# Optimization experiments

Hardware: AMD Instinct MI355X
Metric: run time of the kernel (lower is better)

The kernel has to match this reference:

```python
import jax, jax.numpy as jnp
import numpy as np

P, R, C, K = 128, 256, 256, 3  # nplants, nrows, ncols, kernel_size


def _gconv(x, w, b, groups):
    # x: (1, Cin, R, C); w: (Cout, Cin//groups, K, K); SAME pad == k//2 torch pad for odd k
    y = jax.lax.conv_general_dilated(
        x, w, window_strides=(1, 1), padding='SAME',
        dimension_numbers=('NCHW', 'OIHW', 'NCHW'),
        feature_group_count=groups)
    return y + b[None, :, None, None]


def setup_inputs() -> dict:
    key = jax.random.key(0)
    ks = jax.random.split(key, 10)
    sc = 1.0 / np.sqrt(2 * K * K)  # torch Conv2d default init scale (fan_in = 2*K*K per group)
    return {
        "inputs": jax.random.normal(ks[0], (P, R, C), jnp.float32),
        "prev_state": jax.random.normal(ks[1], (P, R, C), jnp.float32),
        "w_reset": jax.random.uniform(ks[2], (P, 2, K, K), jnp.float32, -sc, sc),
        "b_reset": jax.random.uniform(ks[3], (P,), jnp.float32, -sc, sc),
        "w_update": jax.random.uniform(ks[4], (P, 2, K, K), jnp.float32, -sc, sc),
        "b_update": jax.random.uniform(ks[5], (P,), jnp.float32, -sc, sc),
        "w_out": jax.random.uniform(ks[6], (P, 2, K, K), jnp.float32, -sc, sc),
        "b_out": jax.random.uniform(ks[7], (P,), jnp.float32, -sc, sc),
        # per-pixel reduce weight: Conv2d(R*C*P -> R*C, 1x1, groups=R*C) weight reshaped to (R, C, P)
        "w_read": jax.random.uniform(ks[8], (R, C, P), jnp.float32, -1.0 / np.sqrt(P), 1.0 / np.sqrt(P)),
        "bias": jax.random.normal(ks[9], (R, C), jnp.float32),
    }


def reference(inputs, prev_state, w_reset, b_reset, w_update, b_update,
              w_out, b_out, w_read, bias):
    x = inputs[None]        # (1, P, R, C)
    h = prev_state[None]    # (1, P, R, C)
    stacked = jnp.concatenate([x, h], axis=1)  # (1, 2P, R, C)
    update = jax.nn.sigmoid(_gconv(stacked, w_update, b_update, P))
    reset = jax.nn.sigmoid(_gconv(stacked, w_reset, b_reset, P))
    cand = jnp.tanh(_gconv(jnp.concatenate([x, h * reset], axis=1), w_out, b_out, P))
    new_state = h * (1.0 - update) + cand * update  # (1, P, R, C)
    # grouped 1x1 conv == per-pixel dot over plants
    out = jnp.einsum('prc,rcp->rc', new_state[0], w_read) + bias  # (R, C)
    return out
```

## Files before the change

kernel.cpp:

```cpp
#include <hip/hip_runtime.h>

#define PCNT 128
#define RCdim 256
#define IMG (RCdim*RCdim)
#define PITCH 42
#define TROWS 36
#define TELEMS (TROWS*PITCH)
#define NSLOT 360
#define NTHREADS 256
#define NTASK (34*9)

__device__ __forceinline__ float sig_(float x){ return 1.0f/(1.0f+__expf(-x)); }
__device__ __forceinline__ float th_(float x){ float e=__expf(2.0f*x); return 1.0f-2.0f/(e+1.0f); }

__device__ __forceinline__ void stage4(const float* __restrict__ src, float* __restrict__ dst,
                                       int R0, int C0, int tid){
#pragma unroll
  for (int j=0;j<2;++j){
    int s = j*NTHREADS + tid;
    if (s < NSLOT){
      int rr = s/10, q = s - rr*10;
      int gr = R0-2+rr, gc = C0-4+4*q;
      float4 v = make_float4(0.f,0.f,0.f,0.f);
      if ((unsigned)gr < 256u && (unsigned)gc < 253u)
        v = *(const float4*)(src + gr*RCdim + gc);
      float* d = dst + rr*PITCH + 4*q;
      *(float2*)(d  ) = make_float2(v.x, v.y);
      *(float2*)(d+2) = make_float2(v.z, v.w);
    }
  }
}

__device__ __forceinline__ void load8(const float* __restrict__ T, int row0, int col0, float v[3][8]){
#pragma unroll
  for (int dy=0;dy<3;++dy){
    const float2* p = (const float2*)&T[(row0+dy)*PITCH + col0];
    float2 a=p[0],b=p[1],c=p[2],d=p[3];
    v[dy][0]=a.x; v[dy][1]=a.y; v[dy][2]=b.x; v[dy][3]=b.y;
    v[dy][4]=c.x; v[dy][5]=c.y; v[dy][6]=d.x; v[dy][7]=d.y;
  }
}

template<int OFF>
__device__ __forceinline__ void conv_acc(const float v[3][8], const float w9[9], float o[4]){
#pragma unroll
  for (int ky=0; ky<3; ++ky)
#pragma unroll
    for (int kx=0; kx<3; ++kx){
      const float w = w9[ky*3+kx];
#pragma unroll
      for (int k=0;k<4;++k) o[k] = fmaf(w, v[ky][k+kx+OFF], o[k]);
    }
}

__device__ __forceinline__ void load_w18(const float* __restrict__ g, float w0[9], float w1[9]){
#pragma unroll
  for (int i=0;i<9;++i){ w0[i]=g[i]; w1[i]=g[9+i]; }
}

__device__ __forceinline__ void hr_compute(float (*sm)[TELEMS],
    const float* __restrict__ w_reset, const float* __restrict__ b_reset,
    int a, int tid, float ga[2][4], float gb[2][4]){
  float wr0[9],wr1[9],ws0[9],ws1[9];
  load_w18(w_reset + a*18,     wr0, wr1);
  load_w18(w_reset + (a+1)*18, ws0, ws1);
  const float bra = b_reset[a], brb = b_reset[a+1];
#pragma unroll
  for (int j=0;j<2;++j){
    int sIdx = j*NTHREADS + tid;
    if (sIdx < NTASK){
      int row = sIdx/9, s = sIdx - row*9;
      int rr = row + 1, col0 = 4*s;
      float va[3][8], vb[3][8];
      load8(sm[0], rr-1, col0, va);
      load8(sm[1], rr-1, col0, vb);
      float ra[4] = {bra,bra,bra,bra};
      conv_acc<2>(va, wr0, ra); conv_acc<2>(vb, wr1, ra);
      load8(sm[2], rr-1, col0, va);
      load8(sm[3], rr-1, col0, vb);
      float rb[4] = {brb,brb,brb,brb};
      conv_acc<2>(va, ws0, rb); conv_acc<2>(vb, ws1, rb);
#pragma unroll
      for (int k=0;k<4;++k){ ga[j][k]=sig_(ra[k]); gb[j][k]=sig_(rb[k]); }
    }
  }
}

__device__ __forceinline__ void hr_write(float (*sm)[TELEMS], int tid,
    const float ga[2][4], const float gb[2][4]){
#pragma unroll
  for (int j=0;j<2;++j){
    int sIdx = j*NTHREADS + tid;
    if (sIdx < NTASK){
      int row = sIdx/9, s = sIdx - row*9;
      int rr = row + 1, col0 = 4*s;
      int cnt = (s==8) ? 2 : 4;
      for (int k=0;k<cnt;++k){
        int o = rr*PITCH + col0 + 3 + k;
        sm[0][o] = sm[4][o] * ga[j][k];
        sm[2][o] = sm[5][o] * gb[j][k];
      }
    }
  }
}

__global__ void init_out(const float* __restrict__ bias, float* __restrict__ out){
  int i = blockIdx.x * NTHREADS + threadIdx.x;
  out[i] = bias[i];
}

__global__ void __launch_bounds__(NTHREADS)
reduce_out(const float* __restrict__ ns, const float* __restrict__ w_read,
           const float* __restrict__ bias, float* __restrict__ out){
  const int px = blockIdx.x * NTHREADS + threadIdx.x;
  float acc = bias[px];
  const float* wr = w_read + (size_t)px * PCNT;
#pragma unroll 4
  for (int p0 = 0; p0 < PCNT; p0 += 4){
    const float4 w4 = *(const float4*)&wr[p0];
    acc = fmaf(ns[(size_t)(p0  )*IMG + px], w4.x,
          fmaf(ns[(size_t)(p0+1)*IMG + px], w4.y,
          fmaf(ns[(size_t)(p0+2)*IMG + px], w4.z,
          fmaf(ns[(size_t)(p0+3)*IMG + px], w4.w, acc))));
  }
  out[px] = acc;
}

template<bool SPLIT>
__global__ void __launch_bounds__(NTHREADS, 4)
gru_fused(const float* __restrict__ x, const float* __restrict__ h,
          const float* __restrict__ w_reset, const float* __restrict__ b_reset,
          const float* __restrict__ w_update, const float* __restrict__ b_update,
          const float* __restrict__ w_out, const float* __restrict__ b_out,
          const float* __restrict__ w_read, float* __restrict__ ws,
          float* __restrict__ out)
{
  __shared__ float sm[6][TELEMS];
  const int tid  = threadIdx.x;
  const int bid  = blockIdx.x;
  const int pg   = bid & 15;
  const int tile = bid >> 4;
  const int R0 = (tile >> 3) * 32;
  const int C0 = (tile & 7) * 32;
  const int trow = tid >> 3;
  const int tcol = (tid & 7) * 4;
  const int gidx = (R0 + trow) * RCdim + C0 + tcol;

  float acc[4] = {0.f,0.f,0.f,0.f};
  float v0[3][8], v1[3][8];

#pragma unroll 1
  for (int t = 0; t < 2; ++t){
    const int a  = 4*pg + 2*t;
    const int ph = 64 + 2*pg + t;
    __syncthreads();
    stage4(x + (size_t)(2*a  )*IMG, sm[0], R0,C0,tid);
    stage4(x + (size_t)(2*a+1)*IMG, sm[1], R0,C0,tid);
    stage4(x + (size_t)(2*a+2)*IMG, sm[2], R0,C0,tid);
    stage4(x + (size_t)(2*a+3)*IMG, sm[3], R0,C0,tid);
    stage4(h + (size_t)(a    )*IMG, sm[4], R0,C0,tid);
    stage4(h + (size_t)(a+1  )*IMG, sm[5], R0,C0,tid);
    __syncthreads();

    float hc0[4], hc1[4], uH[4];
    {
      float wa[9], wb[9];
      load_w18(w_update + ph*18, wa, wb);
      const float b = b_update[ph];
      float uo[4] = {b,b,b,b};
      load8(sm[4], trow+1, tcol+2, v0);
      load8(sm[5], trow+1, tcol+2, v1);
      conv_acc<1>(v0, wa, uo); conv_acc<1>(v1, wb, uo);
#pragma unroll
      for (int k=0;k<4;++k){ hc0[k]=v0[1][k+2]; hc1[k]=v1[1][k+2]; uH[k]=sig_(uo[k]); }
    }
    float ns0[4], ns1[4];
    {
      float wua[9],wub[9],woa[9],wob[9];
      load_w18(w_update + a*18, wua, wub);
      load_w18(w_out    + a*18, woa, wob);
      const float bu=b_update[a], bo=b_out[a];
      float uo[4]={bu,bu,bu,bu}, co[4]={bo,bo,bo,bo};
      load8(sm[0], trow+1, tcol+2, v0);
      load8(sm[1], trow+1, tcol+2, v1);
      conv_acc<1>(v0, wua, uo); conv_acc<1>(v1, wub, uo);
      conv_acc<1>(v0, woa, co); conv_acc<1>(v1, wob, co);
#pragma unroll
      for (int k=0;k<4;++k){ float u=sig_(uo[k]); ns0[k]=hc0[k]+u*(th_(co[k])-hc0[k]); }
    }
    {
      float wua[9],wub[9],woa[9],wob[9];
      load_w18(w_update + (a+1)*18, wua, wub);
      load_w18(w_out    + (a+1)*18, woa, wob);
      const float bu=b_update[a+1], bo=b_out[a+1];
      float uo[4]={bu,bu,bu,bu}, co[4]={bo,bo,bo,bo};
      load8(sm[2], trow+1, tcol+2, v0);
      load8(sm[3], trow+1, tcol+2, v1);
      conv_acc<1>(v0, wua, uo); conv_acc<1>(v1, wub, uo);
      conv_acc<1>(v0, woa, co); conv_acc<1>(v1, wob, co);
#pragma unroll
      for (int k=0;k<4;++k){ float u=sig_(uo[k]); ns1[k]=hc1[k]+u*(th_(co[k])-hc1[k]); }
    }
    if (SPLIT){
      *(float4*)&ws[(size_t)a    *IMG + gidx] = make_float4(ns0[0],ns0[1],ns0[2],ns0[3]);
      *(float4*)&ws[(size_t)(a+1)*IMG + gidx] = make_float4(ns1[0],ns1[1],ns1[2],ns1[3]);
    } else {
#pragma unroll
      for (int k=0;k<4;++k){
        const float2 wv = *(const float2*)&w_read[(size_t)(gidx+k)*PCNT + a];
        acc[k] = fmaf(ns0[k], wv.x, fmaf(ns1[k], wv.y, acc[k]));
      }
    }
    float ga[2][4], gb[2][4];
    hr_compute(sm, w_reset, b_reset, a, tid, ga, gb);
    __syncthreads();
    hr_write(sm, tid, ga, gb);
    __syncthreads();
    {
      float woa[9], wob[9];
      load_w18(w_out + ph*18, woa, wob);
      const float bo = b_out[ph];
      float co[4]={bo,bo,bo,bo};
      load8(sm[0], trow+1, tcol+2, v0);
      load8(sm[2], trow+1, tcol+2, v1);
      conv_acc<1>(v0, woa, co); conv_acc<1>(v1, wob, co);
      const float4 hp4 = *(const float4*)&h[(size_t)ph*IMG + gidx];
      const float hp[4] = {hp4.x,hp4.y,hp4.z,hp4.w};
      float nsH[4];
#pragma unroll
      for (int k=0;k<4;++k) nsH[k] = hp[k] + uH[k]*(th_(co[k])-hp[k]);
      if (SPLIT){
        *(float4*)&ws[(size_t)ph*IMG + gidx] = make_float4(nsH[0],nsH[1],nsH[2],nsH[3]);
      } else {
#pragma unroll
        for (int k=0;k<4;++k)
          acc[k] = fmaf(nsH[k], w_read[(size_t)(gidx+k)*PCNT + ph], acc[k]);
      }
    }
  }

#pragma unroll 1
  for (int t = 0; t < 2; ++t){
    const int a    = 64 + 4*pg + 2*t;
    const int ph   = 96 + 2*pg + t;
    const int base = 8*pg + 4*t;
    __syncthreads();
    stage4(h + (size_t)(base  )*IMG, sm[0], R0,C0,tid);
    stage4(h + (size_t)(base+1)*IMG, sm[1], R0,C0,tid);
    stage4(h + (size_t)(base+2)*IMG, sm[2], R0,C0,tid);
    stage4(h + (size_t)(base+3)*IMG, sm[3], R0,C0,tid);
    stage4(h + (size_t)(a     )*IMG, sm[4], R0,C0,tid);
    stage4(h + (size_t)(a+1   )*IMG, sm[5], R0,C0,tid);
    __syncthreads();

    float uH[4];
    {
      float wa[9], wb[9];
      load_w18(w_update + ph*18, wa, wb);
      const float bu = b_update[ph];
      float uo[4] = {bu,bu,bu,bu};
      load8(sm[4], trow+1, tcol+2, v0);
      load8(sm[5], trow+1, tcol+2, v1);
      conv_acc<1>(v0, wa, uo); conv_acc<1>(v1, wb, uo);
#pragma unroll
      for (int k=0;k<4;++k) uH[k]=sig_(uo[k]);
    }
    float ga[2][4], gb[2][4];
    hr_compute(sm, w_reset, b_reset, a, tid, ga, gb);
    __syncthreads();
    hr_write(sm, tid, ga, gb);
    __syncthreads();
    {
      float wa[9], wb[9];
      load_w18(w_out + ph*18, wa, wb);
      const float bo = b_out[ph];
      float co[4] = {bo,bo,bo,bo};
      load8(sm[0], trow+1, tcol+2, v0);
      load8(sm[2], trow+1, tcol+2, v1);
      conv_acc<1>(v0, wa, co); conv_acc<1>(v1, wb, co);
      const float4 hp4 = *(const float4*)&h[(size_t)ph*IMG + gidx];
      const float hp[4] = {hp4.x,hp4.y,hp4.z,hp4.w};
      float nsH[4];
#pragma unroll
      for (int k=0;k<4;++k) nsH[k] = hp[k] + uH[k]*(th_(co[k])-hp[k]);
      if (SPLIT){
        *(float4*)&ws[(size_t)ph*IMG + gidx] = make_float4(nsH[0],nsH[1],nsH[2],nsH[3]);
      } else {
#pragma unroll
        for (int k=0;k<4;++k)
          acc[k] = fmaf(nsH[k], w_read[(size_t)(gidx+k)*PCNT + ph], acc[k]);
      }
    }
  }

  if (!SPLIT){
#pragma unroll
    for (int k=0;k<4;++k) atomicAdd(&out[gidx+k], acc[k]);
  }
}

extern "C" void kernel_launch(void* const* d_in, const int* in_sizes, int n_in,
                              void* d_out, int out_size, void* d_ws, size_t ws_size,
                              hipStream_t stream) {
  const float* x     = (const float*)d_in[0];
  const float* h     = (const float*)d_in[1];
  const float* wrst  = (const float*)d_in[2];
  const float* brst  = (const float*)d_in[3];
  const float* wupd  = (const float*)d_in[4];
  const float* bupd  = (const float*)d_in[5];
  const float* wout  = (const float*)d_in[6];
  const float* bout  = (const float*)d_in[7];
  const float* wread = (const float*)d_in[8];
  const float* bias  = (const float*)d_in[9];
  float* out = (float*)d_out;
  float* ws  = (float*)d_ws;

  const bool split = ws_size >= (size_t)PCNT * IMG * sizeof(float);
  if (split){
    hipLaunchKernelGGL(gru_fused<true>, dim3(64*16), dim3(NTHREADS), 0, stream,
                       x, h, wrst, brst, wupd, bupd, wout, bout, wread, ws, out);
    hipLaunchKernelGGL(reduce_out, dim3(IMG/NTHREADS), dim3(NTHREADS), 0, stream,
                       ws, wread, bias, out);
  } else {
    hipLaunchKernelGGL(init_out, dim3(IMG/NTHREADS), dim3(NTHREADS), 0, stream, bias, out);
    hipLaunchKernelGGL(gru_fused<false>, dim3(64*16), dim3(NTHREADS), 0, stream,
                       x, h, wrst, brst, wupd, bupd, wout, bout, wread, ws, out);
  }
}
```

Before: 66.68 us.

## Restructure GRU tile loop to cut shared memory to four planes and raise occupancy

Merges the two per-plant loops into one four-iteration loop and stages only three planes at a time into four shared buffers instead of six, lowering LDS use so the launch bound can rise from 4 to 6 blocks. The reset convolution is computed directly for each thread's own pixels plus a small halo ring handled by 82 threads, replacing the old strided hr_compute over 306 tasks. The price is extra barriers and a serialized second staging phase inside each iteration, along with more register pressure under the tighter launch bound.

```diff
diff --git a/kernel.cpp b/kernel.cpp
--- a/kernel.cpp
+++ b/kernel.cpp
@@ -8,7 +8,6 @@
 #define TELEMS (TROWS*PITCH)
 #define NSLOT 360
 #define NTHREADS 256
-#define NTASK (34*9)
 
 __device__ __forceinline__ float sig_(float x){ return 1.0f/(1.0f+__expf(-x)); }
 __device__ __forceinline__ float th_(float x){ float e=__expf(2.0f*x); return 1.0f-2.0f/(e+1.0f); }
@@ -57,51 +56,9 @@
 #pragma unroll
   for (int i=0;i<9;++i){ w0[i]=g[i]; w1[i]=g[9+i]; }
 }
-
-__device__ __forceinline__ void hr_compute(float (*sm)[TELEMS],
-    const float* __restrict__ w_reset, const float* __restrict__ b_reset,
-    int a, int tid, float ga[2][4], float gb[2][4]){
-  float wr0[9],wr1[9],ws0[9],ws1[9];
-  load_w18(w_reset + a*18,     wr0, wr1);
-  load_w18(w_reset + (a+1)*18, ws0, ws1);
-  const float bra = b_reset[a], brb = b_reset[a+1];
-#pragma unroll
-  for (int j=0;j<2;++j){
-    int sIdx = j*NTHREADS + tid;
-    if (sIdx < NTASK){
-      int row = sIdx/9, s = sIdx - row*9;
-      int rr = row + 1, col0 = 4*s;
-      float va[3][8], vb[3][8];
-      load8(sm[0], rr-1, col0, va);
-      load8(sm[1], rr-1, col0, vb);
-      float ra[4] = {bra,bra,bra,bra};
-      conv_acc<2>(va, wr0, ra); conv_acc<2>(vb, wr1, ra);
-      load8(sm[2], rr-1, col0, va);
-      load8(sm[3], rr-1, col0, vb);
-      float rb[4] = {brb,brb,brb,brb};
-      conv_acc<2>(va, ws0, rb); conv_acc<2>(vb, ws1, rb);
-#pragma unroll
-      for (int k=0;k<4;++k){ ga[j][k]=sig_(ra[k]); gb[j][k]=sig_(rb[k]); }
-    }
-  }
-}
-
-__device__ __forceinline__ void hr_write(float (*sm)[TELEMS], int tid,
-    const float ga[2][4], const float gb[2][4]){
-#pragma unroll
-  for (int j=0;j<2;++j){
-    int sIdx = j*NTHREADS + tid;
-    if (sIdx < NTASK){
-      int row = sIdx/9, s = sIdx - row*9;
-      int rr = row + 1, col0 = 4*s;
-      int cnt = (s==8) ? 2 : 4;
-      for (int k=0;k<cnt;++k){
-        int o = rr*PITCH + col0 + 3 + k;
-        sm[0][o] = sm[4][o] * ga[j][k];
-        sm[2][o] = sm[5][o] * gb[j][k];
-      }
-    }
-  }
+__device__ __forceinline__ void load_w9(const float* __restrict__ g, float w0[9]){
+#pragma unroll
+  for (int i=0;i<9;++i) w0[i]=g[i];
 }
 
 __global__ void init_out(const float* __restrict__ bias, float* __restrict__ out){
@@ -127,7 +84,7 @@
 }
 
 template<bool SPLIT>
-__global__ void __launch_bounds__(NTHREADS, 4)
+__global__ void __launch_bounds__(NTHREADS, 6)
 gru_fused(const float* __restrict__ x, const float* __restrict__ h,
           const float* __restrict__ w_reset, const float* __restrict__ b_reset,
           const float* __restrict__ w_update, const float* __restrict__ b_update,
@@ -135,7 +92,7 @@
           const float* __restrict__ w_read, float* __restrict__ ws,
           float* __restrict__ out)
 {
-  __shared__ float sm[6][TELEMS];
+  __shared__ float sm[4][TELEMS];
   const int tid  = threadIdx.x;
   const int bid  = blockIdx.x;
   const int pg   = bid & 15;
@@ -146,143 +103,188 @@
   const int tcol = (tid & 7) * 4;
   const int gidx = (R0 + trow) * RCdim + C0 + tcol;
 
+  const bool ringAct = tid < 82;
+  int rrow=1, rwb=2, rk0=0, rkn=0;
+  if (tid < 9)       { rrow = 1;            rwb = 2+4*tid;      rk0 = 0; rkn = (tid==8)?2:4; }
+  else if (tid < 18) { int u=tid-9; rrow=34; rwb = 2+4*u;       rk0 = 0; rkn = (u==8)?2:4; }
+  else if (tid < 50) { rrow = 2+(tid-18);   rwb = 2;            rk0 = 0; rkn = 1; }
+  else if (tid < 82) { rrow = 2+(tid-50);   rwb = 32;           rk0 = 3; rkn = 1; }
+
   float acc[4] = {0.f,0.f,0.f,0.f};
-  float v0[3][8], v1[3][8];
 
 #pragma unroll 1
-  for (int t = 0; t < 2; ++t){
-    const int a  = 4*pg + 2*t;
-    const int ph = 64 + 2*pg + t;
-    __syncthreads();
-    stage4(x + (size_t)(2*a  )*IMG, sm[0], R0,C0,tid);
-    stage4(x + (size_t)(2*a+1)*IMG, sm[1], R0,C0,tid);
-    stage4(x + (size_t)(2*a+2)*IMG, sm[2], R0,C0,tid);
-    stage4(x + (size_t)(2*a+3)*IMG, sm[3], R0,C0,tid);
-    stage4(h + (size_t)(a    )*IMG, sm[4], R0,C0,tid);
-    stage4(h + (size_t)(a+1  )*IMG, sm[5], R0,C0,tid);
-    __syncthreads();
-
-    float hc0[4], hc1[4], uH[4];
-    {
-      float wa[9], wb[9];
-      load_w18(w_update + ph*18, wa, wb);
-      const float b = b_update[ph];
-      float uo[4] = {b,b,b,b};
-      load8(sm[4], trow+1, tcol+2, v0);
-      load8(sm[5], trow+1, tcol+2, v1);
-      conv_acc<1>(v0, wa, uo); conv_acc<1>(v1, wb, uo);
-#pragma unroll
-      for (int k=0;k<4;++k){ hc0[k]=v0[1][k+2]; hc1[k]=v1[1][k+2]; uH[k]=sig_(uo[k]); }
-    }
-    float ns0[4], ns1[4];
-    {
+  for (int it = 0; it < 4; ++it){
+    const bool low = (it < 2);
+    const int t = it & 1;
+    int a, ph;
+    const float *s0, *s1;
+    if (low){
+      a = 4*pg + 2*t; ph = 64 + 2*pg + t;
+      s0 = x + (size_t)(2*a  )*IMG;
+      s1 = x + (size_t)(2*a+2)*IMG;
+    } else {
+      a = 64 + 4*pg + 2*t; ph = 96 + 2*pg + t;
+      const int base = 8*pg + 4*t;
+      s0 = h + (size_t)base*IMG;
+      s1 = h + (size_t)(base+2)*IMG;
+    }
+
+    __syncthreads();
+    stage4(s0,                     sm[0], R0,C0,tid);
+    stage4(s0 + IMG,               sm[1], R0,C0,tid);
+    stage4(h + (size_t)a*IMG,      sm[2], R0,C0,tid);
+    __syncthreads();
+
+    float wr0[9], wr1[9];
+    load_w18(w_reset + a*18, wr0, wr1);
+    const float br0 = b_reset[a];
+
+    float W0[3][8], W1[3][8];
+    load8(sm[0], trow+1, tcol+2, W0);
+    load8(sm[1], trow+1, tcol+2, W1);
+    float ra[4] = {br0,br0,br0,br0};
+    conv_acc<1>(W0, wr0, ra); conv_acc<1>(W1, wr1, ra);
+
+    float upd[4], hc[4];
+    {
+      float wh0[9];
+      load_w9(w_update + ph*18, wh0);
+      const float buh = b_update[ph];
+      float WH[3][8];
+      load8(sm[2], trow+1, tcol+2, WH);
+      upd[0]=buh; upd[1]=buh; upd[2]=buh; upd[3]=buh;
+      conv_acc<1>(WH, wh0, upd);
+#pragma unroll
+      for (int k=0;k<4;++k) hc[k] = WH[1][k+2];
+    }
+
+    if (low){
       float wua[9],wub[9],woa[9],wob[9];
       load_w18(w_update + a*18, wua, wub);
       load_w18(w_out    + a*18, woa, wob);
       const float bu=b_update[a], bo=b_out[a];
       float uo[4]={bu,bu,bu,bu}, co[4]={bo,bo,bo,bo};
-      load8(sm[0], trow+1, tcol+2, v0);
-      load8(sm[1], trow+1, tcol+2, v1);
-      conv_acc<1>(v0, wua, uo); conv_acc<1>(v1, wub, uo);
-      conv_acc<1>(v0, woa, co); conv_acc<1>(v1, wob, co);
-#pragma unroll
-      for (int k=0;k<4;++k){ float u=sig_(uo[k]); ns0[k]=hc0[k]+u*(th_(co[k])-hc0[k]); }
-    }
-    {
+      conv_acc<1>(W0, wua, uo); conv_acc<1>(W1, wub, uo);
+      conv_acc<1>(W0, woa, co); conv_acc<1>(W1, wob, co);
+      float ns0[4];
+#pragma unroll
+      for (int k=0;k<4;++k){ float u=sig_(uo[k]); ns0[k]=hc[k]+u*(th_(co[k])-hc[k]); }
+      if (SPLIT){
+        *(float4*)&ws[(size_t)a*IMG + gidx] = make_float4(ns0[0],ns0[1],ns0[2],ns0[3]);
+      } else {
+#pragma unroll
+        for (int k=0;k<4;++k)
+          acc[k] = fmaf(ns0[k], w_read[(size_t)(gidx+k)*PCNT + a], acc[k]);
+      }
+    }
+
+    float rsig[4];
+    if (ringAct){
+      float rv0[3][8], rv1[3][8];
+      load8(sm[0], rrow-1, rwb, rv0);
+      load8(sm[1], rrow-1, rwb, rv1);
+      float rr[4] = {br0,br0,br0,br0};
+      conv_acc<0>(rv0, wr0, rr); conv_acc<0>(rv1, wr1, rr);
+#pragma unroll
+      for (int k=0;k<4;++k) rsig[k] = sig_(rr[k]);
+    }
+    __syncthreads();
+
+    stage4(s1,                      sm[0], R0,C0,tid);
+    stage4(s1 + IMG,                sm[1], R0,C0,tid);
+    stage4(h + (size_t)(a+1)*IMG,   sm[3], R0,C0,tid);
+    {
+      float* d = &sm[2][(trow+2)*PITCH + tcol+4];
+      *(float2*)(d  ) = make_float2(hc[0]*sig_(ra[0]), hc[1]*sig_(ra[1]));
+      *(float2*)(d+2) = make_float2(hc[2]*sig_(ra[2]), hc[3]*sig_(ra[3]));
+    }
+    if (ringAct){
+      for (int k=rk0; k<rk0+rkn; ++k){
+        int o = rrow*PITCH + rwb+1+k;
+        sm[2][o] = sm[2][o] * rsig[k];
+      }
+    }
+    __syncthreads();
+
+    load_w18(w_reset + (a+1)*18, wr0, wr1);
+    const float br1 = b_reset[a+1];
+    load8(sm[0], trow+1, tcol+2, W0);
+    load8(sm[1], trow+1, tcol+2, W1);
+    float ra2[4] = {br1,br1,br1,br1};
+    conv_acc<1>(W0, wr0, ra2); conv_acc<1>(W1, wr1, ra2);
+
+    float hc2[4];
+    {
+      float wh1[9];
+      load_w9(w_update + ph*18 + 9, wh1);
+      float WH[3][8];
+      load8(sm[3], trow+1, tcol+2, WH);
+      conv_acc<1>(WH, wh1, upd);
+#pragma unroll
+      for (int k=0;k<4;++k) hc2[k] = WH[1][k+2];
+    }
+
+    if (low){
       float wua[9],wub[9],woa[9],wob[9];
       load_w18(w_update + (a+1)*18, wua, wub);
       load_w18(w_out    + (a+1)*18, woa, wob);
       const float bu=b_update[a+1], bo=b_out[a+1];
       float uo[4]={bu,bu,bu,bu}, co[4]={bo,bo,bo,bo};
-      load8(sm[2], trow+1, tcol+2, v0);
-      load8(sm[3], trow+1, tcol+2, v1);
-      conv_acc<1>(v0, wua, uo); conv_acc<1>(v1, wub, uo);
-      conv_acc<1>(v0, woa, co); conv_acc<1>(v1, wob, co);
-#pragma unroll
-      for (int k=0;k<4;++k){ float u=sig_(uo[k]); ns1[k]=hc1[k]+u*(th_(co[k])-hc1[k]); }
-    }
-    if (SPLIT){
-      *(float4*)&ws[(size_t)a    *IMG + gidx] = make_float4(ns0[0],ns0[1],ns0[2],ns0[3]);
-      *(float4*)&ws[(size_t)(a+1)*IMG + gidx] = make_float4(ns1[0],ns1[1],ns1[2],ns1[3]);
-    } else {
-#pragma unroll
-      for (int k=0;k<4;++k){
-        const float2 wv = *(const float2*)&w_read[(size_t)(gidx+k)*PCNT + a];
-        acc[k] = fmaf(ns0[k], wv.x, fmaf(ns1[k], wv.y, acc[k]));
-      }
-    }
-    float ga[2][4], gb[2][4];
-    hr_compute(sm, w_reset, b_reset, a, tid, ga, gb);
-    __syncthreads();
-    hr_write(sm, tid, ga, gb);
-    __syncthreads();
-    {
-      float woa[9], wob[9];
-      load_w18(w_out + ph*18, woa, wob);
+      conv_acc<1>(W0, wua, uo); conv_acc<1>(W1, wub, uo);
+      conv_acc<1>(W0, woa, co); conv_acc<1>(W1, wob, co);
+      float ns1[4];
+#pragma unroll
+      for (int k=0;k<4;++k){ float u=sig_(uo[k]); ns1[k]=hc2[k]+u*(th_(co[k])-hc2[k]); }
+      if (SPLIT){
+        *(float4*)&ws[(size_t)(a+1)*IMG + gidx] = make_float4(ns1[0],ns1[1],ns1[2],ns1[3]);
+      } else {
+#pragma unroll
+        for (int k=0;k<4;++k)
+          acc[k] = fmaf(ns1[k], w_read[(size_t)(gidx+k)*PCNT + (a+1)], acc[k]);
+      }
+    }
+
+    float rsig2[4];
+    if (ringAct){
+      float rv0[3][8], rv1[3][8];
+      load8(sm[0], rrow-1, rwb, rv0);
+      load8(sm[1], rrow-1, rwb, rv1);
+      float rr[4] = {br1,br1,br1,br1};
+      conv_acc<0>(rv0, wr0, rr); conv_acc<0>(rv1, wr1, rr);
+#pragma unroll
+      for (int k=0;k<4;++k) rsig2[k] = sig_(rr[k]);
+    }
+    __syncthreads();
+
+    {
+      float* d = &sm[3][(trow+2)*PITCH + tcol+4];
+      *(float2*)(d  ) = make_float2(hc2[0]*sig_(ra2[0]), hc2[1]*sig_(ra2[1]));
+      *(float2*)(d+2) = make_float2(hc2[2]*sig_(ra2[2]), hc2[3]*sig_(ra2[3]));
+    }
+    if (ringAct){
+      for (int k=rk0; k<rk0+rkn; ++k){
+        int o = rrow*PITCH + rwb+1+k;
+        sm[3][o] = sm[3][o] * rsig2[k];
+      }
+    }
+    __syncthreads();
+
+    {
+      float woh0[9], woh1[9];
+      load_w18(w_out + ph*18, woh0, woh1);
       const float bo = b_out[ph];
       float co[4]={bo,bo,bo,bo};
-      load8(sm[0], trow+1, tcol+2, v0);
-      load8(sm[2], trow+1, tcol+2, v1);
-      conv_acc<1>(v0, woa, co); conv_acc<1>(v1, wob, co);
+      load8(sm[2], trow+1, tcol+2, W0);
+      load8(sm[3], trow+1, tcol+2, W1);
+      conv_acc<1>(W0, woh0, co); conv_acc<1>(W1, woh1, co);
       const float4 hp4 = *(const float4*)&h[(size_t)ph*IMG + gidx];
       const float hp[4] = {hp4.x,hp4.y,hp4.z,hp4.w};
       float nsH[4];
 #pragma unroll
-      for (int k=0;k<4;++k) nsH[k] = hp[k] + uH[k]*(th_(co[k])-hp[k]);
-      if (SPLIT){
-        *(float4*)&ws[(size_t)ph*IMG + gidx] = make_float4(nsH[0],nsH[1],nsH[2],nsH[3]);
-      } else {
-#pragma unroll
-        for (int k=0;k<4;++k)
-          acc[k] = fmaf(nsH[k], w_read[(size_t)(gidx+k)*PCNT + ph], acc[k]);
-      }
-    }
-  }
-
-#pragma unroll 1
-  for (int t = 0; t < 2; ++t){
-    const int a    = 64 + 4*pg + 2*t;
-    const int ph   = 96 + 2*pg + t;
-    const int base = 8*pg + 4*t;
-    __syncthreads();
-    stage4(h + (size_t)(base  )*IMG, sm[0], R0,C0,tid);
-    stage4(h + (size_t)(base+1)*IMG, sm[1], R0,C0,tid);
-    stage4(h + (size_t)(base+2)*IMG, sm[2], R0,C0,tid);
-    stage4(h + (size_t)(base+3)*IMG, sm[3], R0,C0,tid);
-    stage4(h + (size_t)(a     )*IMG, sm[4], R0,C0,tid);
-    stage4(h + (size_t)(a+1   )*IMG, sm[5], R0,C0,tid);
-    __syncthreads();
-
-    float uH[4];
-    {
-      float wa[9], wb[9];
-      load_w18(w_update + ph*18, wa, wb);
-      const float bu = b_update[ph];
-      float uo[4] = {bu,bu,bu,bu};
-      load8(sm[4], trow+1, tcol+2, v0);
-      load8(sm[5], trow+1, tcol+2, v1);
-      conv_acc<1>(v0, wa, uo); conv_acc<1>(v1, wb, uo);
-#pragma unroll
-      for (int k=0;k<4;++k) uH[k]=sig_(uo[k]);
-    }
-    float ga[2][4], gb[2][4];
-    hr_compute(sm, w_reset, b_reset, a, tid, ga, gb);
-    __syncthreads();
-    hr_write(sm, tid, ga, gb);
-    __syncthreads();
-    {
-      float wa[9], wb[9];
-      load_w18(w_out + ph*18, wa, wb);
-      const float bo = b_out[ph];
-      float co[4] = {bo,bo,bo,bo};
-      load8(sm[0], trow+1, tcol+2, v0);
-      load8(sm[2], trow+1, tcol+2, v1);
-      conv_acc<1>(v0, wa, co); conv_acc<1>(v1, wb, co);
-      const float4 hp4 = *(const float4*)&h[(size_t)ph*IMG + gidx];
-      const float hp[4] = {hp4.x,hp4.y,hp4.z,hp4.w};
-      float nsH[4];
-#pragma unroll
-      for (int k=0;k<4;++k) nsH[k] = hp[k] + uH[k]*(th_(co[k])-hp[k]);
+      for (int k=0;k<4;++k){
+        float u = sig_(upd[k]);
+        nsH[k] = hp[k] + u*(th_(co[k])-hp[k]);
+      }
       if (SPLIT){
         *(float4*)&ws[(size_t)ph*IMG + gidx] = make_float4(nsH[0],nsH[1],nsH[2],nsH[3]);
       } else {
```

After: 165.8 us. 2.49x slower.
